# Kernel tuning notes

Measured on AMD Instinct MI355X. Metric: run time of the kernel, lower is better.

Reference implementation:

```python
import jax, jax.numpy as jnp
import numpy as np

P = 2.0  # exponent from init kwarg p


def _segment_mean(vals, idx, n):
    # scatter-mean with zero for empty segments (matches torch_scatter reduce='mean')
    s = jax.ops.segment_sum(vals, idx, num_segments=n)
    c = jax.ops.segment_sum(jnp.ones((vals.shape[0], 1), vals.dtype), idx, num_segments=n)
    return s / jnp.maximum(c, 1.0)


def setup_inputs() -> dict:
    key = jax.random.key(0)
    ks = jax.random.split(key, 6)
    N, E, nhid, heads = 100000, 3200000, 64, 4
    X = jax.random.normal(ks[0], (N, nhid), dtype=jnp.float32)
    edge_index = jax.random.randint(ks[1], (2, E), 0, N, dtype=jnp.int32)
    s1 = 1.0 / np.sqrt(nhid)
    W_self = jax.random.normal(ks[2], (nhid, nhid), dtype=jnp.float32) * s1
    W_neigh = jax.random.normal(ks[3], (nhid, nhid), dtype=jnp.float32) * s1
    b_conv = jnp.zeros((nhid,), dtype=jnp.float32)
    s2 = 1.0 / np.sqrt(2 * nhid)
    Qw = jax.random.normal(ks[4], (heads, 2 * nhid, nhid // heads), dtype=jnp.float32) * s2
    Qb = jnp.zeros((heads, nhid // heads), dtype=jnp.float32)
    return {"X": X, "edge_index": edge_index, "W_self": W_self,
            "W_neigh": W_neigh, "b_conv": b_conv, "Qw": Qw, "Qb": Qb}


def reference(X, edge_index, W_self, W_neigh, b_conv, Qw, Qb):
    N = X.shape[0]
    src, dst = edge_index[0], edge_index[1]
    # GraphSAGE conv: self-linear + linear over mean of neighbor features, then ReLU
    agg = _segment_mean(X[src], dst, N)                     # [N, nhid]
    X2 = jax.nn.relu(X @ W_self + agg @ W_neigh + b_conv)   # [N, nhid]
    # gather both edge endpoints and concat
    ef = jnp.concatenate([X2[src], X2[dst]], axis=1)        # [E, 2*nhid]
    # per-head small linear, abs^p, heads concatenated -> [E, nhid]
    h = jnp.einsum('ef,hfd->ehd', ef, Qw) + Qb              # [E, heads, nhid/heads]
    h = (jnp.abs(h) ** P).reshape(ef.shape[0], -1)
    # scatter-mean by source node, tanh
    gg = jnp.tanh(_segment_mean(h, src, N))                 # [N, nhid]
    return gg
```

## Files before the change

### kernel.cpp

```cpp
#include <hip/hip_runtime.h>
#include <math.h>

#define NHID 64
#define NPB 512
#define NPB_SHIFT 9
#define MAXB 256
#define CAP 20480
#define CHUNK 8192

__device__ __forceinline__ float bf_lo(unsigned u) { return __uint_as_float(u << 16); }
__device__ __forceinline__ float bf_hi(unsigned u) { return __uint_as_float(u & 0xffff0000u); }
__device__ __forceinline__ unsigned f2bf(float f) {
    unsigned u = __float_as_uint(f);
    return (u + 0x7fffu + ((u >> 16) & 1u)) >> 16;
}

__global__ __launch_bounds__(256) void k_bucketA(const int* __restrict__ src,
                                                 const int* __restrict__ dst,
                                                 unsigned int* __restrict__ buf0,
                                                 unsigned int* __restrict__ buf1,
                                                 int* __restrict__ btail0,
                                                 int* __restrict__ btail1,
                                                 int E, int nB) {
    int side  = blockIdx.x & 1;
    int chunk = blockIdx.x >> 1;
    const int* key = side ? src : dst;
    const int* pay = side ? dst : src;
    unsigned int* buf = side ? buf1 : buf0;
    int* btail = side ? btail1 : btail0;

    __shared__ int h[MAXB], b[MAXB];
    int tid = threadIdx.x;
    for (int i = tid; i < nB; i += 256) h[i] = 0;
    __syncthreads();
    int e0 = chunk * CHUNK;
    for (int i = tid; i < CHUNK / 4; i += 256) {
        int e = e0 + i * 4;
        if (e + 3 < E) {
            int4 k4 = ((const int4*)(key + e0))[i];
            atomicAdd(&h[k4.x >> NPB_SHIFT], 1);
            atomicAdd(&h[k4.y >> NPB_SHIFT], 1);
            atomicAdd(&h[k4.z >> NPB_SHIFT], 1);
            atomicAdd(&h[k4.w >> NPB_SHIFT], 1);
        } else {
            for (int j = 0; j < 4; ++j) {
                int e2 = e + j;
                if (e2 < E) atomicAdd(&h[key[e2] >> NPB_SHIFT], 1);
            }
        }
    }
    __syncthreads();
    for (int i = tid; i < nB; i += 256) {
        int c = h[i];
        b[i] = c ? atomicAdd(&btail[i], c) : 0;
        h[i] = 0;
    }
    __syncthreads();
    for (int i = tid; i < CHUNK / 4; i += 256) {
        int e = e0 + i * 4;
        if (e + 3 < E) {
            int4 k4 = ((const int4*)(key + e0))[i];
            int4 p4 = ((const int4*)(pay + e0))[i];
            int bb, r;
            bb = k4.x >> NPB_SHIFT; r = atomicAdd(&h[bb], 1) + b[bb];
            if (r < CAP) buf[(size_t)bb * CAP + r] = ((unsigned)p4.x << NPB_SHIFT) | (unsigned)(k4.x & (NPB - 1));
            bb = k4.y >> NPB_SHIFT; r = atomicAdd(&h[bb], 1) + b[bb];
            if (r < CAP) buf[(size_t)bb * CAP + r] = ((unsigned)p4.y << NPB_SHIFT) | (unsigned)(k4.y & (NPB - 1));
            bb = k4.z >> NPB_SHIFT; r = atomicAdd(&h[bb], 1) + b[bb];
            if (r < CAP) buf[(size_t)bb * CAP + r] = ((unsigned)p4.z << NPB_SHIFT) | (unsigned)(k4.z & (NPB - 1));
            bb = k4.w >> NPB_SHIFT; r = atomicAdd(&h[bb], 1) + b[bb];
            if (r < CAP) buf[(size_t)bb * CAP + r] = ((unsigned)p4.w << NPB_SHIFT) | (unsigned)(k4.w & (NPB - 1));
        } else {
            for (int j = 0; j < 4; ++j) {
                int e2 = e + j;
                if (e2 < E) {
                    int k = key[e2], p = pay[e2];
                    int bb = k >> NPB_SHIFT;
                    int r = atomicAdd(&h[bb], 1) + b[bb];
                    if (r < CAP) buf[(size_t)bb * CAP + r] = ((unsigned)p << NPB_SHIFT) | (unsigned)(k & (NPB - 1));
                }
            }
        }
    }
}

__global__ __launch_bounds__(256) void k_bscan(const int* __restrict__ btail0,
                                               const int* __restrict__ btail1,
                                               int* __restrict__ boff0, int* __restrict__ boff1,
                                               int* __restrict__ off0, int* __restrict__ off1,
                                               int nB, int N) {
    __shared__ int sd[256];
    int tid = threadIdx.x;
    int v = (tid < nB) ? min(btail0[tid], CAP) : 0;
    sd[tid] = v; __syncthreads();
    for (int o = 1; o < 256; o <<= 1) {
        int t = (tid >= o) ? sd[tid - o] : 0; __syncthreads();
        sd[tid] += t; __syncthreads();
    }
    if (tid < nB) boff0[tid] = sd[tid] - v;
    if (tid == 255) off0[N] = sd[255];
    __syncthreads();
    v = (tid < nB) ? min(btail1[tid], CAP) : 0;
    sd[tid] = v; __syncthreads();
    for (int o = 1; o < 256; o <<= 1) {
        int t = (tid >= o) ? sd[tid - o] : 0; __syncthreads();
        sd[tid] += t; __syncthreads();
    }
    if (tid < nB) boff1[tid] = sd[tid] - v;
    if (tid == 255) off1[N] = sd[255];
}

__global__ __launch_bounds__(512) void k_bucket_csr(const unsigned int* __restrict__ buf0,
                                                    const unsigned int* __restrict__ buf1,
                                                    const int* __restrict__ btail0,
                                                    const int* __restrict__ btail1,
                                                    const int* __restrict__ boff0,
                                                    const int* __restrict__ boff1,
                                                    int* __restrict__ off0, int* __restrict__ off1,
                                                    int* __restrict__ csr0, int* __restrict__ csr1,
                                                    int N) {
    int side = blockIdx.x & 1;
    int b = blockIdx.x >> 1;
    const unsigned int* buf = (side ? buf1 : buf0) + (size_t)b * CAP;
    int cnt_b = min((side ? btail1 : btail0)[b], CAP);
    int boff  = (side ? boff1 : boff0)[b];
    int* off  = side ? off1 : off0;
    int* csr  = side ? csr1 : csr0;
    __shared__ int cnt[NPB];
    __shared__ int scn[NPB];
    __shared__ int cur[NPB];
    int tid = threadIdx.x;
    cnt[tid] = 0;
    __syncthreads();
    for (int i = tid; i < cnt_b; i += 512)
        atomicAdd(&cnt[buf[i] & (NPB - 1)], 1);
    __syncthreads();
    int v = cnt[tid];
    scn[tid] = v; __syncthreads();
    for (int o = 1; o < 512; o <<= 1) {
        int t = (tid >= o) ? scn[tid - o] : 0; __syncthreads();
        scn[tid] += t; __syncthreads();
    }
    int base = boff + scn[tid] - v;
    cur[tid] = base;
    int node = (b << NPB_SHIFT) + tid;
    if (node < N) off[node] = base;
    __syncthreads();
    for (int i = tid; i < cnt_b; i += 512) {
        unsigned int u = buf[i];
        int pos = atomicAdd(&cur[u & (NPB - 1)], 1);
        csr[pos] = (int)(u >> NPB_SHIFT);
    }
}

__global__ __launch_bounds__(256) void k_xcast(const float* __restrict__ X,
                                               unsigned* __restrict__ Xb, int total8) {
    int i = blockIdx.x * 256 + threadIdx.x;
    if (i >= total8) return;
    const float4* Xv = (const float4*)X;
    float4 f0 = Xv[(size_t)i * 2];
    float4 f1 = Xv[(size_t)i * 2 + 1];
    uint4 p;
    p.x = f2bf(f0.x) | (f2bf(f0.y) << 16);
    p.y = f2bf(f0.z) | (f2bf(f0.w) << 16);
    p.z = f2bf(f1.x) | (f2bf(f1.y) << 16);
    p.w = f2bf(f1.z) | (f2bf(f1.w) << 16);
    ((uint4*)Xb)[i] = p;
}

#define AGG_ACC(u) \
    accA.x += bf_lo(u.x); accA.y += bf_hi(u.x); \
    accA.z += bf_lo(u.y); accA.w += bf_hi(u.y); \
    accB.x += bf_lo(u.z); accB.y += bf_hi(u.z); \
    accB.z += bf_lo(u.w); accB.w += bf_hi(u.w);
#define AGG_ACCM(u, f) \
    accA.x += f * bf_lo(u.x); accA.y += f * bf_hi(u.x); \
    accA.z += f * bf_lo(u.y); accA.w += f * bf_hi(u.y); \
    accB.x += f * bf_lo(u.z); accB.y += f * bf_hi(u.z); \
    accB.z += f * bf_lo(u.w); accB.w += f * bf_hi(u.w);

__global__ __launch_bounds__(256) void k_agg(const unsigned* __restrict__ Xb,
                                             const int* __restrict__ off_dst,
                                             const int* __restrict__ csr_dst,
                                             float* __restrict__ agg, int N) {
    int lane = threadIdx.x & 63;
    int node = blockIdx.x * 4 + (threadIdx.x >> 6);
    if (node >= N) return;
    int grp = lane >> 3, col8 = lane & 7;
    const uint4* Xb4 = (const uint4*)Xb;
    int s0 = off_dst[node], s1 = off_dst[node + 1];
    float4 accA = make_float4(0.f, 0.f, 0.f, 0.f);
    float4 accB = make_float4(0.f, 0.f, 0.f, 0.f);
    for (int base = s0; base < s1; base += 64) {
        int cnt = min(64, s1 - base);
        int idx = (base + lane < s1) ? csr_dst[base + lane] : 0;
        int j = 0;
        for (; j + 32 <= cnt; j += 32) {
            int m0 = __shfl(idx, j + grp);
            int m1 = __shfl(idx, j + 8 + grp);
            int m2 = __shfl(idx, j + 16 + grp);
            int m3 = __shfl(idx, j + 24 + grp);
            uint4 u0 = Xb4[(size_t)m0 * 8 + col8];
            uint4 u1 = Xb4[(size_t)m1 * 8 + col8];
            uint4 u2 = Xb4[(size_t)m2 * 8 + col8];
            uint4 u3 = Xb4[(size_t)m3 * 8 + col8];
            AGG_ACC(u0); AGG_ACC(u1); AGG_ACC(u2); AGG_ACC(u3);
        }
        if (j < cnt) {
            int q0 = j + grp, q1 = j + 8 + grp, q2 = j + 16 + grp, q3 = j + 24 + grp;
            int m0 = __shfl(idx, q0);
            int m1 = __shfl(idx, q1);
            int m2 = __shfl(idx, q2);
            int m3 = __shfl(idx, q3);
            float f0 = (q0 < cnt) ? 1.f : 0.f; if (q0 >= cnt) m0 = 0;
            float f1 = (q1 < cnt) ? 1.f : 0.f; if (q1 >= cnt) m1 = 0;
            float f2 = (q2 < cnt) ? 1.f : 0.f; if (q2 >= cnt) m2 = 0;
            float f3 = (q3 < cnt) ? 1.f : 0.f; if (q3 >= cnt) m3 = 0;
            uint4 u0 = Xb4[(size_t)m0 * 8 + col8];
            uint4 u1 = Xb4[(size_t)m1 * 8 + col8];
            uint4 u2 = Xb4[(size_t)m2 * 8 + col8];
            uint4 u3 = Xb4[(size_t)m3 * 8 + col8];
            AGG_ACCM(u0, f0); AGG_ACCM(u1, f1); AGG_ACCM(u2, f2); AGG_ACCM(u3, f3);
        }
    }
    #pragma unroll
    for (int d = 8; d < 64; d <<= 1) {
        accA.x += __shfl_xor(accA.x, d); accA.y += __shfl_xor(accA.y, d);
        accA.z += __shfl_xor(accA.z, d); accA.w += __shfl_xor(accA.w, d);
        accB.x += __shfl_xor(accB.x, d); accB.y += __shfl_xor(accB.y, d);
        accB.z += __shfl_xor(accB.z, d); accB.w += __shfl_xor(accB.w, d);
    }
    if (grp == 0) {
        int deg = s1 - s0;
        float inv = 1.f / (float)max(deg, 1);
        float4 r0 = make_float4(accA.x * inv, accA.y * inv, accA.z * inv, accA.w * inv);
        float4 r1 = make_float4(accB.x * inv, accB.y * inv, accB.z * inv, accB.w * inv);
        ((float4*)agg)[(size_t)node * 16 + col8 * 2]     = r0;
        ((float4*)agg)[(size_t)node * 16 + col8 * 2 + 1] = r1;
    }
}

__global__ __launch_bounds__(256) void k_phaseA(const float* __restrict__ X,
                                                const float* __restrict__ agg,
                                                const float* __restrict__ Ws,
                                                const float* __restrict__ Wn,
                                                const float* __restrict__ bconv,
                                                unsigned* __restrict__ X2b, int N) {
    __shared__ float sWs[4096];
    __shared__ float sWn[4096];
    __shared__ float sb[64];
    int tid = threadIdx.x;
    for (int i = tid; i < 4096; i += 256) {
        sWs[i] = Ws[i];
        sWn[i] = Wn[i];
    }
    if (tid < 64) sb[tid] = bconv[tid];
    __syncthreads();

    int n = blockIdx.x * 64 + (tid >> 2);
    if (n >= N) return;
    int wb = (tid & 3) << 2;
    const float4* ws4 = (const float4*)sWs;
    const float4* wn4 = (const float4*)sWn;
    const float4* bv  = (const float4*)sb;
    const float4* Xv  = (const float4*)(X + (size_t)n * NHID);
    const float4* Gv  = (const float4*)(agg + (size_t)n * NHID);
    float4 a0 = bv[wb], a1 = bv[wb + 1], a2 = bv[wb + 2], a3 = bv[wb + 3];
    #pragma unroll 2
    for (int q = 0; q < 16; ++q) {
        float4 xq = Xv[q];
        float4 gq = Gv[q];
        float xs[4] = {xq.x, xq.y, xq.z, xq.w};
        float gs[4] = {gq.x, gq.y, gq.z, gq.w};
        #pragma unroll
        for (int j = 0; j < 4; ++j) {
            int k16 = (4 * q + j) * 16 + wb;
            float4 w0 = ws4[k16], w1 = ws4[k16 + 1], w2 = ws4[k16 + 2], w3 = ws4[k16 + 3];
            float4 m0 = wn4[k16], m1 = wn4[k16 + 1], m2 = wn4[k16 + 2], m3 = wn4[k16 + 3];
            float xj = xs[j], gj = gs[j];
            a0.x += xj * w0.x + gj * m0.x; a0.y += xj * w0.y + gj * m0.y;
            a0.z += xj * w0.z + gj * m0.z; a0.w += xj * w0.w + gj * m0.w;
            a1.x += xj * w1.x + gj * m1.x; a1.y += xj * w1.y + gj * m1.y;
            a1.z += xj * w1.z + gj * m1.z; a1.w += xj * w1.w + gj * m1.w;
            a2.x += xj * w2.x + gj * m2.x; a2.y += xj * w2.y + gj * m2.y;
            a2.z += xj * w2.z + gj * m2.z; a2.w += xj * w2.w + gj * m2.w;
            a3.x += xj * w3.x + gj * m3.x; a3.y += xj * w3.y + gj * m3.y;
            a3.z += xj * w3.z + gj * m3.z; a3.w += xj * w3.w + gj * m3.w;
        }
    }
    a0.x = fmaxf(a0.x, 0.f); a0.y = fmaxf(a0.y, 0.f); a0.z = fmaxf(a0.z, 0.f); a0.w = fmaxf(a0.w, 0.f);
    a1.x = fmaxf(a1.x, 0.f); a1.y = fmaxf(a1.y, 0.f); a1.z = fmaxf(a1.z, 0.f); a1.w = fmaxf(a1.w, 0.f);
    a2.x = fmaxf(a2.x, 0.f); a2.y = fmaxf(a2.y, 0.f); a2.z = fmaxf(a2.z, 0.f); a2.w = fmaxf(a2.w, 0.f);
    a3.x = fmaxf(a3.x, 0.f); a3.y = fmaxf(a3.y, 0.f); a3.z = fmaxf(a3.z, 0.f); a3.w = fmaxf(a3.w, 0.f);
    uint4 p0, p1;
    p0.x = f2bf(a0.x) | (f2bf(a0.y) << 16);
    p0.y = f2bf(a0.z) | (f2bf(a0.w) << 16);
    p0.z = f2bf(a1.x) | (f2bf(a1.y) << 16);
    p0.w = f2bf(a1.z) | (f2bf(a1.w) << 16);
    p1.x = f2bf(a2.x) | (f2bf(a2.y) << 16);
    p1.y = f2bf(a2.z) | (f2bf(a2.w) << 16);
    p1.z = f2bf(a3.x) | (f2bf(a3.y) << 16);
    p1.w = f2bf(a3.z) | (f2bf(a3.w) << 16);
    uint4* outp = (uint4*)X2b + (size_t)n * 8 + (tid & 3) * 2;
    outp[0] = p0; outp[1] = p1;
}

__global__ __launch_bounds__(256) void k_repackB(const float* __restrict__ Qw,
                                                 float* __restrict__ W2) {
    int i = blockIdx.x * 256 + threadIdx.x;
    if (i >= 8192) return;
    int f = i >> 7, c = i & 127;
    float v;
    if (c < 64) v = Qw[(c >> 4) * 2048 + f * 16 + (c & 15)];
    else { int cc = c - 64; v = Qw[(cc >> 4) * 2048 + (64 + f) * 16 + (cc & 15)]; }
    W2[i] = v;
}

__global__ __launch_bounds__(256) void k_phaseB(const unsigned* __restrict__ X2b,
                                                const float* __restrict__ W2,
                                                const float* __restrict__ Qb,
                                                unsigned* __restrict__ aOut,
                                                unsigned* __restrict__ bOut, int N) {
    __shared__ float sW[8192];
    int tid = threadIdx.x;
    for (int i = tid; i < 8192; i += 256) sW[i] = W2[i];
    __syncthreads();

    int n = blockIdx.x * 32 + (tid >> 3);
    if (n >= N) return;
    int part = tid & 7;
    int wb = part << 2;
    const float4* w4 = (const float4*)sW;
    float4 a0, a1, a2, a3;
    if (part < 4) {
        const float4* qv = (const float4*)Qb;
        a0 = qv[wb]; a1 = qv[wb + 1]; a2 = qv[wb + 2]; a3 = qv[wb + 3];
    } else {
        a0 = a1 = a2 = a3 = make_float4(0.f, 0.f, 0.f, 0.f);
    }
    const uint4* Xv = (const uint4*)((const uint4*)X2b + (size_t)n * 8);
    #pragma unroll 2
    for (int q8 = 0; q8 < 8; ++q8) {
        uint4 xu = Xv[q8];
        float xs[8] = {bf_lo(xu.x), bf_hi(xu.x), bf_lo(xu.y), bf_hi(xu.y),
                       bf_lo(xu.z), bf_hi(xu.z), bf_lo(xu.w), bf_hi(xu.w)};
        #pragma unroll
        for (int j = 0; j < 8; ++j) {
            int f32b = (8 * q8 + j) * 32 + wb;
            float4 w0 = w4[f32b], w1 = w4[f32b + 1], w2 = w4[f32b + 2], w3 = w4[f32b + 3];
            float xj = xs[j];
            a0.x += xj * w0.x; a0.y += xj * w0.y; a0.z += xj * w0.z; a0.w += xj * w0.w;
            a1.x += xj * w1.x; a1.y += xj * w1.y; a1.z += xj * w1.z; a1.w += xj * w1.w;
            a2.x += xj * w2.x; a2.y += xj * w2.y; a2.z += xj * w2.z; a2.w += xj * w2.w;
            a3.x += xj * w3.x; a3.y += xj * w3.y; a3.z += xj * w3.z; a3.w += xj * w3.w;
        }
    }
    uint4 p0, p1;
    p0.x = f2bf(a0.x) | (f2bf(a0.y) << 16);
    p0.y = f2bf(a0.z) | (f2bf(a0.w) << 16);
    p0.z = f2bf(a1.x) | (f2bf(a1.y) << 16);
    p0.w = f2bf(a1.z) | (f2bf(a1.w) << 16);
    p1.x = f2bf(a2.x) | (f2bf(a2.y) << 16);
    p1.y = f2bf(a2.z) | (f2bf(a2.w) << 16);
    p1.z = f2bf(a3.x) | (f2bf(a3.y) << 16);
    p1.w = f2bf(a3.z) | (f2bf(a3.w) << 16);
    uint4* outp = (part < 4) ? (uint4*)aOut + (size_t)n * 8 + part * 2
                             : (uint4*)bOut + (size_t)n * 8 + (part - 4) * 2;
    outp[0] = p0; outp[1] = p1;
}

#define FIN_ACC(u) { float t; \
    t = avA.x + bf_lo(u.x); accA.x += t * t; \
    t = avA.y + bf_hi(u.x); accA.y += t * t; \
    t = avA.z + bf_lo(u.y); accA.z += t * t; \
    t = avA.w + bf_hi(u.y); accA.w += t * t; \
    t = avB.x + bf_lo(u.z); accB.x += t * t; \
    t = avB.y + bf_hi(u.z); accB.y += t * t; \
    t = avB.z + bf_lo(u.w); accB.z += t * t; \
    t = avB.w + bf_hi(u.w); accB.w += t * t; }
#define FIN_ACCM(u, f) { float t; \
    t = avA.x + bf_lo(u.x); accA.x += f * t * t; \
    t = avA.y + bf_hi(u.x); accA.y += f * t * t; \
    t = avA.z + bf_lo(u.y); accA.z += f * t * t; \
    t = avA.w + bf_hi(u.y); accA.w += f * t * t; \
    t = avB.x + bf_lo(u.z); accB.x += f * t * t; \
    t = avB.y + bf_hi(u.z); accB.y += f * t * t; \
    t = avB.z + bf_lo(u.w); accB.z += f * t * t; \
    t = avB.w + bf_hi(u.w); accB.w += f * t * t; }

__global__ __launch_bounds__(256) void k_final(const unsigned* __restrict__ aFb,
                                               const unsigned* __restrict__ bFb,
                                               const int* __restrict__ off_src,
                                               const int* __restrict__ csr_src,
                                               float* __restrict__ out, int N) {
    int lane = threadIdx.x & 63;
    int node = blockIdx.x * 4 + (threadIdx.x >> 6);
    if (node >= N) return;
    int grp = lane >> 3, col8 = lane & 7;
    const uint4* Bv = (const uint4*)bFb;
    uint4 au = ((const uint4*)aFb)[(size_t)node * 8 + col8];
    float4 avA = make_float4(bf_lo(au.x), bf_hi(au.x), bf_lo(au.y), bf_hi(au.y));
    float4 avB = make_float4(bf_lo(au.z), bf_hi(au.z), bf_lo(au.w), bf_hi(au.w));
    int s0 = off_src[node], s1 = off_src[node + 1];
    float4 accA = make_float4(0.f, 0.f, 0.f, 0.f);
    float4 accB = make_float4(0.f, 0.f, 0.f, 0.f);
    for (int base = s0; base < s1; base += 64) {
        int cnt = min(64, s1 - base);
        int idx = (base + lane < s1) ? csr_src[base + lane] : 0;
        int j = 0;
        for (; j + 32 <= cnt; j += 32) {
            int m0 = __shfl(idx, j + grp);
            int m1 = __shfl(idx, j + 8 + grp);
            int m2 = __shfl(idx, j + 16 + grp);
            int m3 = __shfl(idx, j + 24 + grp);
            uint4 u0 = Bv[(size_t)m0 * 8 + col8];
            uint4 u1 = Bv[(size_t)m1 * 8 + col8];
            uint4 u2 = Bv[(size_t)m2 * 8 + col8];
            uint4 u3 = Bv[(size_t)m3 * 8 + col8];
            FIN_ACC(u0); FIN_ACC(u1); FIN_ACC(u2); FIN_ACC(u3);
        }
        if (j < cnt) {
            int q0 = j + grp, q1 = j + 8 + grp, q2 = j + 16 + grp, q3 = j + 24 + grp;
            int m0 = __shfl(idx, q0);
            int m1 = __shfl(idx, q1);
            int m2 = __shfl(idx, q2);
            int m3 = __shfl(idx, q3);
            float f0 = (q0 < cnt) ? 1.f : 0.f; if (q0 >= cnt) m0 = 0;
            float f1 = (q1 < cnt) ? 1.f : 0.f; if (q1 >= cnt) m1 = 0;
            float f2 = (q2 < cnt) ? 1.f : 0.f; if (q2 >= cnt) m2 = 0;
            float f3 = (q3 < cnt) ? 1.f : 0.f; if (q3 >= cnt) m3 = 0;
            uint4 u0 = Bv[(size_t)m0 * 8 + col8];
            uint4 u1 = Bv[(size_t)m1 * 8 + col8];
            uint4 u2 = Bv[(size_t)m2 * 8 + col8];
            uint4 u3 = Bv[(size_t)m3 * 8 + col8];
            FIN_ACCM(u0, f0); FIN_ACCM(u1, f1); FIN_ACCM(u2, f2); FIN_ACCM(u3, f3);
        }
    }
    #pragma unroll
    for (int d = 8; d < 64; d <<= 1) {
        accA.x += __shfl_xor(accA.x, d); accA.y += __shfl_xor(accA.y, d);
        accA.z += __shfl_xor(accA.z, d); accA.w += __shfl_xor(accA.w, d);
        accB.x += __shfl_xor(accB.x, d); accB.y += __shfl_xor(accB.y, d);
        accB.z += __shfl_xor(accB.z, d); accB.w += __shfl_xor(accB.w, d);
    }
    if (grp == 0) {
        int deg = s1 - s0;
        float inv = 1.f / (float)max(deg, 1);
        float4 r0 = make_float4(tanhf(accA.x * inv), tanhf(accA.y * inv),
                                tanhf(accA.z * inv), tanhf(accA.w * inv));
        float4 r1 = make_float4(tanhf(accB.x * inv), tanhf(accB.y * inv),
                                tanhf(accB.z * inv), tanhf(accB.w * inv));
        ((float4*)out)[(size_t)node * 16 + col8 * 2]     = r0;
        ((float4*)out)[(size_t)node * 16 + col8 * 2 + 1] = r1;
    }
}

extern "C" void kernel_launch(void* const* d_in, const int* in_sizes, int n_in,
                              void* d_out, int out_size, void* d_ws, size_t ws_size,
                              hipStream_t stream) {
    const float* X      = (const float*)d_in[0];
    const int*   ei     = (const int*)d_in[1];
    const float* Wself  = (const float*)d_in[2];
    const float* Wneigh = (const float*)d_in[3];
    const float* bconv  = (const float*)d_in[4];
    const float* Qw     = (const float*)d_in[5];
    const float* Qb     = (const float*)d_in[6];

    int N = in_sizes[0] / NHID;
    int E = in_sizes[1] / 2;
    const int* src = ei;
    const int* dst = ei + E;
    int nB = (N + NPB - 1) >> NPB_SHIFT;
    int nChunks = (E + CHUNK - 1) / CHUNK;

    char* ws = (char*)d_ws;
    size_t bufBytes = (size_t)MAXB * CAP * 4;
    size_t NH4 = (size_t)N * NHID * 4;
    size_t NH2 = (size_t)N * NHID * 2;
    unsigned int* buf0 = (unsigned int*)(ws);
    unsigned int* buf1 = (unsigned int*)(ws + bufBytes);
    float*    aggF = (float*)(ws);
    unsigned* X2b  = (unsigned*)(ws + NH4);
    unsigned* aFb  = (unsigned*)(ws + NH4 + NH2);
    unsigned* bFb  = (unsigned*)(ws + NH4 + 2 * NH2);
    unsigned* Xb   = (unsigned*)(ws + NH4 + 3 * NH2);
    size_t pos = NH4 + 4 * NH2;
    if (pos < 2 * bufBytes) pos = 2 * bufBytes;
    pos = (pos + 255) & ~(size_t)255;
    auto alloc = [&](size_t bytes) -> void* {
        void* p = ws + pos;
        pos = (pos + bytes + 255) & ~(size_t)255;
        return p;
    };
    int* csr0   = (int*)alloc((size_t)E * 4);
    int* csr1   = (int*)alloc((size_t)E * 4);
    int* off0   = (int*)alloc((size_t)(N + 1) * 4);
    int* off1   = (int*)alloc((size_t)(N + 1) * 4);
    int* btail0 = (int*)alloc((size_t)MAXB * 4);
    int* btail1 = (int*)alloc((size_t)MAXB * 4);
    int* boff0  = (int*)alloc((size_t)MAXB * 4);
    int* boff1  = (int*)alloc((size_t)MAXB * 4);
    float* W2   = (float*)alloc((size_t)8192 * 4);
    (void)ws_size; (void)n_in; (void)out_size;

    hipMemsetAsync(btail0, 0, (size_t)2 * MAXB * 4, stream);

    k_bucketA<<<nChunks * 2, 256, 0, stream>>>(src, dst, buf0, buf1, btail0, btail1, E, nB);
    k_bscan<<<1, 256, 0, stream>>>(btail0, btail1, boff0, boff1, off0, off1, nB, N);
    k_repackB<<<32, 256, 0, stream>>>(Qw, W2);
    k_xcast<<<(N * 8 + 255) / 256, 256, 0, stream>>>(X, Xb, N * 8);
    k_bucket_csr<<<nB * 2, 512, 0, stream>>>(buf0, buf1, btail0, btail1,
                                             boff0, boff1, off0, off1, csr0, csr1, N);
    k_agg<<<(N + 3) / 4, 256, 0, stream>>>(Xb, off0, csr0, aggF, N);
    k_phaseA<<<(N + 63) / 64, 256, 0, stream>>>(X, aggF, Wself, Wneigh, bconv, X2b, N);
    k_phaseB<<<(N + 31) / 32, 256, 0, stream>>>(X2b, W2, Qb, aFb, bFb, N);
    k_final<<<(N + 3) / 4, 256, 0, stream>>>(aFb, bFb, off1, csr1, (float*)d_out, N);
}
```

Baseline: 329.6 us.

## Split gather tables into four column partitions for cache-resident neighbor aggregation

The bf16 feature tables (Xb, aFb, bFb) are now stored as four column-slabs of 16 features each, and the two gather-heavy kernels (neighbor mean and final scatter-mean) run as four passes, one per slab. Each pass gathers 32 bytes per node from a 3.2 MB table instead of 128 bytes from a 12.8 MB table, so the randomly accessed working set may stay in L2/MALL. The cost is four times the launches, and the CSR offsets and indices are re-read once per pass.

```diff
diff --git a/kernel.cpp b/kernel.cpp
--- a/kernel.cpp
+++ b/kernel.cpp
@@ -154,89 +154,74 @@
 }
 
 __global__ __launch_bounds__(256) void k_xcast(const float* __restrict__ X,
-                                               unsigned* __restrict__ Xb, int total8) {
+                                               unsigned* __restrict__ Xb, int N) {
     int i = blockIdx.x * 256 + threadIdx.x;
-    if (i >= total8) return;
-    const float4* Xv = (const float4*)X;
-    float4 f0 = Xv[(size_t)i * 2];
-    float4 f1 = Xv[(size_t)i * 2 + 1];
-    uint4 p;
-    p.x = f2bf(f0.x) | (f2bf(f0.y) << 16);
-    p.y = f2bf(f0.z) | (f2bf(f0.w) << 16);
-    p.z = f2bf(f1.x) | (f2bf(f1.y) << 16);
-    p.w = f2bf(f1.z) | (f2bf(f1.w) << 16);
-    ((uint4*)Xb)[i] = p;
-}
-
-#define AGG_ACC(u) \
-    accA.x += bf_lo(u.x); accA.y += bf_hi(u.x); \
-    accA.z += bf_lo(u.y); accA.w += bf_hi(u.y); \
-    accB.x += bf_lo(u.z); accB.y += bf_hi(u.z); \
-    accB.z += bf_lo(u.w); accB.w += bf_hi(u.w);
-#define AGG_ACCM(u, f) \
-    accA.x += f * bf_lo(u.x); accA.y += f * bf_hi(u.x); \
-    accA.z += f * bf_lo(u.y); accA.w += f * bf_hi(u.y); \
-    accB.x += f * bf_lo(u.z); accB.y += f * bf_hi(u.z); \
-    accB.z += f * bf_lo(u.w); accB.w += f * bf_hi(u.w);
-
-__global__ __launch_bounds__(256) void k_agg(const unsigned* __restrict__ Xb,
-                                             const int* __restrict__ off_dst,
-                                             const int* __restrict__ csr_dst,
-                                             float* __restrict__ agg, int N) {
+    if (i >= N * 4) return;
+    int n = i >> 2, p = i & 3;
+    const float4* Xv = (const float4*)(X + (size_t)n * NHID + p * 16);
+    float4 f0 = Xv[0], f1 = Xv[1], f2 = Xv[2], f3 = Xv[3];
+    uint4 a, c;
+    a.x = f2bf(f0.x) | (f2bf(f0.y) << 16);
+    a.y = f2bf(f0.z) | (f2bf(f0.w) << 16);
+    a.z = f2bf(f1.x) | (f2bf(f1.y) << 16);
+    a.w = f2bf(f1.z) | (f2bf(f1.w) << 16);
+    c.x = f2bf(f2.x) | (f2bf(f2.y) << 16);
+    c.y = f2bf(f2.z) | (f2bf(f2.w) << 16);
+    c.z = f2bf(f3.x) | (f2bf(f3.y) << 16);
+    c.w = f2bf(f3.z) | (f2bf(f3.w) << 16);
+    uint4* d = (uint4*)Xb + ((size_t)p * N + n) * 2;
+    d[0] = a; d[1] = c;
+}
+
+__global__ __launch_bounds__(256) void k_agg_p(const unsigned* __restrict__ Xbp,
+                                               const int* __restrict__ off_dst,
+                                               const int* __restrict__ csr_dst,
+                                               float* __restrict__ agg, int N, int part) {
     int lane = threadIdx.x & 63;
     int node = blockIdx.x * 4 + (threadIdx.x >> 6);
     if (node >= N) return;
-    int grp = lane >> 3, col8 = lane & 7;
-    const uint4* Xb4 = (const uint4*)Xb;
+    int grp = lane >> 2, col4 = lane & 3;
+    const uint2* T = (const uint2*)Xbp;
     int s0 = off_dst[node], s1 = off_dst[node + 1];
-    float4 accA = make_float4(0.f, 0.f, 0.f, 0.f);
-    float4 accB = make_float4(0.f, 0.f, 0.f, 0.f);
+    float4 acc = make_float4(0.f, 0.f, 0.f, 0.f);
     for (int base = s0; base < s1; base += 64) {
         int cnt = min(64, s1 - base);
         int idx = (base + lane < s1) ? csr_dst[base + lane] : 0;
         int j = 0;
         for (; j + 32 <= cnt; j += 32) {
             int m0 = __shfl(idx, j + grp);
-            int m1 = __shfl(idx, j + 8 + grp);
-            int m2 = __shfl(idx, j + 16 + grp);
-            int m3 = __shfl(idx, j + 24 + grp);
-            uint4 u0 = Xb4[(size_t)m0 * 8 + col8];
-            uint4 u1 = Xb4[(size_t)m1 * 8 + col8];
-            uint4 u2 = Xb4[(size_t)m2 * 8 + col8];
-            uint4 u3 = Xb4[(size_t)m3 * 8 + col8];
-            AGG_ACC(u0); AGG_ACC(u1); AGG_ACC(u2); AGG_ACC(u3);
+            int m1 = __shfl(idx, j + 16 + grp);
+            uint2 u0 = T[(size_t)m0 * 4 + col4];
+            uint2 u1 = T[(size_t)m1 * 4 + col4];
+            acc.x += bf_lo(u0.x); acc.y += bf_hi(u0.x);
+            acc.z += bf_lo(u0.y); acc.w += bf_hi(u0.y);
+            acc.x += bf_lo(u1.x); acc.y += bf_hi(u1.x);
+            acc.z += bf_lo(u1.y); acc.w += bf_hi(u1.y);
         }
         if (j < cnt) {
-            int q0 = j + grp, q1 = j + 8 + grp, q2 = j + 16 + grp, q3 = j + 24 + grp;
+            int q0 = j + grp, q1 = j + 16 + grp;
             int m0 = __shfl(idx, q0);
             int m1 = __shfl(idx, q1);
-            int m2 = __shfl(idx, q2);
-            int m3 = __shfl(idx, q3);
             float f0 = (q0 < cnt) ? 1.f : 0.f; if (q0 >= cnt) m0 = 0;
             float f1 = (q1 < cnt) ? 1.f : 0.f; if (q1 >= cnt) m1 = 0;
-            float f2 = (q2 < cnt) ? 1.f : 0.f; if (q2 >= cnt) m2 = 0;
-            float f3 = (q3 < cnt) ? 1.f : 0.f; if (q3 >= cnt) m3 = 0;
-            uint4 u0 = Xb4[(size_t)m0 * 8 + col8];
-            uint4 u1 = Xb4[(size_t)m1 * 8 + col8];
-            uint4 u2 = Xb4[(size_t)m2 * 8 + col8];
-            uint4 u3 = Xb4[(size_t)m3 * 8 + col8];
-            AGG_ACCM(u0, f0); AGG_ACCM(u1, f1); AGG_ACCM(u2, f2); AGG_ACCM(u3, f3);
+            uint2 u0 = T[(size_t)m0 * 4 + col4];
+            uint2 u1 = T[(size_t)m1 * 4 + col4];
+            acc.x += f0 * bf_lo(u0.x); acc.y += f0 * bf_hi(u0.x);
+            acc.z += f0 * bf_lo(u0.y); acc.w += f0 * bf_hi(u0.y);
+            acc.x += f1 * bf_lo(u1.x); acc.y += f1 * bf_hi(u1.x);
+            acc.z += f1 * bf_lo(u1.y); acc.w += f1 * bf_hi(u1.y);
         }
     }
     #pragma unroll
-    for (int d = 8; d < 64; d <<= 1) {
-        accA.x += __shfl_xor(accA.x, d); accA.y += __shfl_xor(accA.y, d);
-        accA.z += __shfl_xor(accA.z, d); accA.w += __shfl_xor(accA.w, d);
-        accB.x += __shfl_xor(accB.x, d); accB.y += __shfl_xor(accB.y, d);
-        accB.z += __shfl_xor(accB.z, d); accB.w += __shfl_xor(accB.w, d);
+    for (int d = 4; d < 64; d <<= 1) {
+        acc.x += __shfl_xor(acc.x, d); acc.y += __shfl_xor(acc.y, d);
+        acc.z += __shfl_xor(acc.z, d); acc.w += __shfl_xor(acc.w, d);
     }
     if (grp == 0) {
         int deg = s1 - s0;
         float inv = 1.f / (float)max(deg, 1);
-        float4 r0 = make_float4(accA.x * inv, accA.y * inv, accA.z * inv, accA.w * inv);
-        float4 r1 = make_float4(accB.x * inv, accB.y * inv, accB.z * inv, accB.w * inv);
-        ((float4*)agg)[(size_t)node * 16 + col8 * 2]     = r0;
-        ((float4*)agg)[(size_t)node * 16 + col8 * 2 + 1] = r1;
+        ((float4*)agg)[(size_t)node * 16 + part * 4 + col4] =
+            make_float4(acc.x * inv, acc.y * inv, acc.z * inv, acc.w * inv);
     }
 }
 
@@ -338,7 +323,7 @@
     } else {
         a0 = a1 = a2 = a3 = make_float4(0.f, 0.f, 0.f, 0.f);
     }
-    const uint4* Xv = (const uint4*)((const uint4*)X2b + (size_t)n * 8);
+    const uint4* Xv = (const uint4*)X2b + (size_t)n * 8;
     #pragma unroll 2
     for (int q8 = 0; q8 < 8; ++q8) {
         uint4 xu = Xv[q8];
@@ -364,94 +349,74 @@
     p1.y = f2bf(a2.z) | (f2bf(a2.w) << 16);
     p1.z = f2bf(a3.x) | (f2bf(a3.y) << 16);
     p1.w = f2bf(a3.z) | (f2bf(a3.w) << 16);
-    uint4* outp = (part < 4) ? (uint4*)aOut + (size_t)n * 8 + part * 2
-                             : (uint4*)bOut + (size_t)n * 8 + (part - 4) * 2;
+    uint4* outp = (part < 4) ? (uint4*)aOut + ((size_t)part * N + n) * 2
+                             : (uint4*)bOut + ((size_t)(part - 4) * N + n) * 2;
     outp[0] = p0; outp[1] = p1;
 }
 
-#define FIN_ACC(u) { float t; \
-    t = avA.x + bf_lo(u.x); accA.x += t * t; \
-    t = avA.y + bf_hi(u.x); accA.y += t * t; \
-    t = avA.z + bf_lo(u.y); accA.z += t * t; \
-    t = avA.w + bf_hi(u.y); accA.w += t * t; \
-    t = avB.x + bf_lo(u.z); accB.x += t * t; \
-    t = avB.y + bf_hi(u.z); accB.y += t * t; \
-    t = avB.z + bf_lo(u.w); accB.z += t * t; \
-    t = avB.w + bf_hi(u.w); accB.w += t * t; }
-#define FIN_ACCM(u, f) { float t; \
-    t = avA.x + bf_lo(u.x); accA.x += f * t * t; \
-    t = avA.y + bf_hi(u.x); accA.y += f * t * t; \
-    t = avA.z + bf_lo(u.y); accA.z += f * t * t; \
-    t = avA.w + bf_hi(u.y); accA.w += f * t * t; \
-    t = avB.x + bf_lo(u.z); accB.x += f * t * t; \
-    t = avB.y + bf_hi(u.z); accB.y += f * t * t; \
-    t = avB.z + bf_lo(u.w); accB.z += f * t * t; \
-    t = avB.w + bf_hi(u.w); accB.w += f * t * t; }
-
-__global__ __launch_bounds__(256) void k_final(const unsigned* __restrict__ aFb,
-                                               const unsigned* __restrict__ bFb,
-                                               const int* __restrict__ off_src,
-                                               const int* __restrict__ csr_src,
-                                               float* __restrict__ out, int N) {
+__global__ __launch_bounds__(256) void k_final_p(const unsigned* __restrict__ aFb,
+                                                 const unsigned* __restrict__ bFb,
+                                                 const int* __restrict__ off_src,
+                                                 const int* __restrict__ csr_src,
+                                                 float* __restrict__ out, int N, int part) {
     int lane = threadIdx.x & 63;
     int node = blockIdx.x * 4 + (threadIdx.x >> 6);
     if (node >= N) return;
-    int grp = lane >> 3, col8 = lane & 7;
-    const uint4* Bv = (const uint4*)bFb;
-    uint4 au = ((const uint4*)aFb)[(size_t)node * 8 + col8];
-    float4 avA = make_float4(bf_lo(au.x), bf_hi(au.x), bf_lo(au.y), bf_hi(au.y));
-    float4 avB = make_float4(bf_lo(au.z), bf_hi(au.z), bf_lo(au.w), bf_hi(au.w));
+    int grp = lane >> 2, col4 = lane & 3;
+    const uint2* T = (const uint2*)bFb + (size_t)part * N * 4;
+    uint2 au = ((const uint2*)aFb)[((size_t)part * N + node) * 4 + col4];
+    float4 av = make_float4(bf_lo(au.x), bf_hi(au.x), bf_lo(au.y), bf_hi(au.y));
     int s0 = off_src[node], s1 = off_src[node + 1];
-    float4 accA = make_float4(0.f, 0.f, 0.f, 0.f);
-    float4 accB = make_float4(0.f, 0.f, 0.f, 0.f);
+    float4 acc = make_float4(0.f, 0.f, 0.f, 0.f);
     for (int base = s0; base < s1; base += 64) {
         int cnt = min(64, s1 - base);
         int idx = (base + lane < s1) ? csr_src[base + lane] : 0;
         int j = 0;
         for (; j + 32 <= cnt; j += 32) {
             int m0 = __shfl(idx, j + grp);
-            int m1 = __shfl(idx, j + 8 + grp);
-            int m2 = __shfl(idx, j + 16 + grp);
-            int m3 = __shfl(idx, j + 24 + grp);
-            uint4 u0 = Bv[(size_t)m0 * 8 + col8];
-            uint4 u1 = Bv[(size_t)m1 * 8 + col8];
-            uint4 u2 = Bv[(size_t)m2 * 8 + col8];
-            uint4 u3 = Bv[(size_t)m3 * 8 + col8];
-            FIN_ACC(u0); FIN_ACC(u1); FIN_ACC(u2); FIN_ACC(u3);
+            int m1 = __shfl(idx, j + 16 + grp);
+            uint2 u0 = T[(size_t)m0 * 4 + col4];
+            uint2 u1 = T[(size_t)m1 * 4 + col4];
+            float t;
+            t = av.x + bf_lo(u0.x); acc.x += t * t;
+            t = av.y + bf_hi(u0.x); acc.y += t * t;
+            t = av.z + bf_lo(u0.y); acc.z += t * t;
+            t = av.w + bf_hi(u0.y); acc.w += t * t;
+            t = av.x + bf_lo(u1.x); acc.x += t * t;
+            t = av.y + bf_hi(u1.x); acc.y += t * t;
+            t = av.z + bf_lo(u1.y); acc.z += t * t;
+            t = av.w + bf_hi(u1.y); acc.w += t * t;
         }
         if (j < cnt) {
-            int q0 = j + grp, q1 = j + 8 + grp, q2 = j + 16 + grp, q3 = j + 24 + grp;
+            int q0 = j + grp, q1 = j + 16 + grp;
             int m0 = __shfl(idx, q0);
             int m1 = __shfl(idx, q1);
-            int m2 = __shfl(idx, q2);
-            int m3 = __shfl(idx, q3);
             float f0 = (q0 < cnt) ? 1.f : 0.f; if (q0 >= cnt) m0 = 0;
             float f1 = (q1 < cnt) ? 1.f : 0.f; if (q1 >= cnt) m1 = 0;
-            float f2 = (q2 < cnt) ? 1.f : 0.f; if (q2 >= cnt) m2 = 0;
-            float f3 = (q3 < cnt) ? 1.f : 0.f; if (q3 >= cnt) m3 = 0;
-            uint4 u0 = Bv[(size_t)m0 * 8 + col8];
-            uint4 u1 = Bv[(size_t)m1 * 8 + col8];
-            uint4 u2 = Bv[(size_t)m2 * 8 + col8];
-            uint4 u3 = Bv[(size_t)m3 * 8 + col8];
-            FIN_ACCM(u0, f0); FIN_ACCM(u1, f1); FIN_ACCM(u2, f2); FIN_ACCM(u3, f3);
+            uint2 u0 = T[(size_t)m0 * 4 + col4];
+            uint2 u1 = T[(size_t)m1 * 4 + col4];
+            float t;
+            t = av.x + bf_lo(u0.x); acc.x += f0 * t * t;
+            t = av.y + bf_hi(u0.x); acc.y += f0 * t * t;
+            t = av.z + bf_lo(u0.y); acc.z += f0 * t * t;
+            t = av.w + bf_hi(u0.y); acc.w += f0 * t * t;
+            t = av.x + bf_lo(u1.x); acc.x += f1 * t * t;
+            t = av.y + bf_hi(u1.x); acc.y += f1 * t * t;
+            t = av.z + bf_lo(u1.y); acc.z += f1 * t * t;
+            t = av.w + bf_hi(u1.y); acc.w += f1 * t * t;
         }
     }
     #pragma unroll
-    for (int d = 8; d < 64; d <<= 1) {
-        accA.x += __shfl_xor(accA.x, d); accA.y += __shfl_xor(accA.y, d);
-        accA.z += __shfl_xor(accA.z, d); accA.w += __shfl_xor(accA.w, d);
-        accB.x += __shfl_xor(accB.x, d); accB.y += __shfl_xor(accB.y, d);
-        accB.z += __shfl_xor(accB.z, d); accB.w += __shfl_xor(accB.w, d);
+    for (int d = 4; d < 64; d <<= 1) {
+        acc.x += __shfl_xor(acc.x, d); acc.y += __shfl_xor(acc.y, d);
+        acc.z += __shfl_xor(acc.z, d); acc.w += __shfl_xor(acc.w, d);
     }
     if (grp == 0) {
         int deg = s1 - s0;
         float inv = 1.f / (float)max(deg, 1);
-        float4 r0 = make_float4(tanhf(accA.x * inv), tanhf(accA.y * inv),
-                                tanhf(accA.z * inv), tanhf(accA.w * inv));
-        float4 r1 = make_float4(tanhf(accB.x * inv), tanhf(accB.y * inv),
-                                tanhf(accB.z * inv), tanhf(accB.w * inv));
-        ((float4*)out)[(size_t)node * 16 + col8 * 2]     = r0;
-        ((float4*)out)[(size_t)node * 16 + col8 * 2 + 1] = r1;
+        ((float4*)out)[(size_t)node * 16 + part * 4 + col4] =
+            make_float4(tanhf(acc.x * inv), tanhf(acc.y * inv),
+                        tanhf(acc.z * inv), tanhf(acc.w * inv));
     }
 }
 
@@ -508,11 +473,15 @@
     k_bucketA<<<nChunks * 2, 256, 0, stream>>>(src, dst, buf0, buf1, btail0, btail1, E, nB);
     k_bscan<<<1, 256, 0, stream>>>(btail0, btail1, boff0, boff1, off0, off1, nB, N);
     k_repackB<<<32, 256, 0, stream>>>(Qw, W2);
-    k_xcast<<<(N * 8 + 255) / 256, 256, 0, stream>>>(X, Xb, N * 8);
+    k_xcast<<<(N * 4 + 255) / 256, 256, 0, stream>>>(X, Xb, N);
     k_bucket_csr<<<nB * 2, 512, 0, stream>>>(buf0, buf1, btail0, btail1,
                                              boff0, boff1, off0, off1, csr0, csr1, N);
-    k_agg<<<(N + 3) / 4, 256, 0, stream>>>(Xb, off0, csr0, aggF, N);
+    for (int p = 0; p < 4; ++p)
+        k_agg_p<<<(N + 3) / 4, 256, 0, stream>>>(Xb + (size_t)p * N * 8, off0, csr0,
+                                                 aggF, N, p);
     k_phaseA<<<(N + 63) / 64, 256, 0, stream>>>(X, aggF, Wself, Wneigh, bconv, X2b, N);
     k_phaseB<<<(N + 31) / 32, 256, 0, stream>>>(X2b, W2, Qb, aFb, bFb, N);
-    k_final<<<(N + 3) / 4, 256, 0, stream>>>(aFb, bFb, off1, csr1, (float*)d_out, N);
-}
+    for (int p = 0; p < 4; ++p)
+        k_final_p<<<(N + 3) / 4, 256, 0, stream>>>(aFb, bFb, off1, csr1,
+                                                   (float*)d_out, N, p);
+}
```

After: 498.1 us. 1.51x slower.
